# Kernel optimization log

Hardware: AMD Instinct MI355X
Metric: run time of the kernel (lower is better)

Reference implementation:

```python
import math
import jax, jax.numpy as jnp
import numpy as np

B, T, D, H = 2, 2048, 1024, 16
HD = D // H
LN_EPS = 1e-5


def new_gelu(x):
    c = math.sqrt(2.0 / math.pi)
    return 0.5 * x * (1.0 + jnp.tanh(c * (x + 0.044715 * x * x * x)))


def layer_norm(x, w, b):
    mu = jnp.mean(x, axis=-1, keepdims=True)
    var = jnp.var(x, axis=-1, keepdims=True)
    return (x - mu) * jax.lax.rsqrt(var + LN_EPS) * w + b


def setup_inputs() -> dict:
    key = jax.random.key(0)
    ks = jax.random.split(key, 9)
    s = 0.02
    return {
        "x": jax.random.normal(ks[0], (B, T, D), jnp.float32),
        "wq": jax.random.normal(ks[1], (D, D), jnp.float32) * s,
        "wk": jax.random.normal(ks[2], (D, D), jnp.float32) * s,
        "wv": jax.random.normal(ks[3], (D, D), jnp.float32) * s,
        "Er": jax.random.normal(ks[4], (H, T, HD), jnp.float32),
        "fc1_w": jax.random.normal(ks[5], (4 * D, D), jnp.float32) * s,
        "fc1_b": jax.random.normal(ks[6], (4 * D,), jnp.float32) * s,
        "fc2_w": jax.random.normal(ks[7], (D, 4 * D), jnp.float32) * s,
        "fc2_b": jax.random.normal(ks[8], (D,), jnp.float32) * s,
        "ln1_w": jnp.ones((D,), jnp.float32),
        "ln1_b": jnp.zeros((D,), jnp.float32),
        "ln2_w": jnp.ones((D,), jnp.float32),
        "ln2_b": jnp.zeros((D,), jnp.float32),
    }


def rel_attention(x, wq, wk, wv, Er):
    b, t, c = x.shape
    # torch nn.Linear: y = x @ W^T  (weights stored [out, in])
    q = (x @ wq.T).reshape(b, t, H, HD).transpose(0, 2, 1, 3)  # [B,H,T,HD]
    k = (x @ wk.T).reshape(b, t, H, HD).transpose(0, 2, 1, 3)
    v = (x @ wv.T).reshape(b, t, H, HD).transpose(0, 2, 1, 3)

    raw_attn = jnp.einsum("bhqd,bhkd->bhqk", q, k)  # [B,H,T,T]
    # relative-position logits + skew trick
    srel = jnp.einsum("bhqd,hrd->bhqr", q, Er[:, -t:, :])  # [B,H,T,T]
    srel = jnp.pad(srel, ((0, 0), (0, 0), (0, 0), (1, 0)))  # [B,H,T,T+1]
    srel = srel.reshape(b, H, t + 1, t)[:, :, 1:, :]  # skewed [B,H,T,T]

    attn = (raw_attn + srel) * (1.0 / math.sqrt(HD))
    causal = jnp.tril(jnp.ones((t, t), bool))
    attn = jnp.where(causal[None, None], attn, -jnp.inf)
    attn = jax.nn.softmax(attn, axis=-1)

    y = jnp.einsum("bhqk,bhkd->bhqd", attn, v)
    return y.transpose(0, 2, 1, 3).reshape(b, t, c)


def reference(x, wq, wk, wv, Er, fc1_w, fc1_b, fc2_w, fc2_b, ln1_w, ln1_b, ln2_w, ln2_b):
    x = x + rel_attention(layer_norm(x, ln1_w, ln1_b), wq, wk, wv, Er)
    h = layer_norm(x, ln2_w, ln2_b)
    h = new_gelu(h @ fc1_w.T + fc1_b)
    x = x + (h @ fc2_w.T + fc2_b)
    return x
```

## Files before the change

kernel.cpp:

```cpp
#include <hip/hip_runtime.h>
#include <hip/hip_bf16.h>

#define Bb 2
#define Tt 2048
#define Dd 1024
#define Hh 16

typedef short s16x8 __attribute__((ext_vector_type(8)));
typedef float f32x4 __attribute__((ext_vector_type(4)));
typedef unsigned short u16;
typedef short mfma_in_t __attribute__((ext_vector_type(8)));

typedef const __attribute__((address_space(1))) void gvoid;
typedef __attribute__((address_space(3))) void lvoid;

__device__ inline u16 f2bf(float f) {
  union { float f; unsigned u; } v; v.f = f;
  unsigned r = v.u + 0x7FFF + ((v.u >> 16) & 1);
  return (u16)(r >> 16);
}
__device__ inline u16 f2bf_t(float f) {
  return (u16)(__builtin_bit_cast(unsigned, f) >> 16);
}
__device__ inline float bf2f(u16 v) {
  return __builtin_bit_cast(float, (unsigned)v << 16);
}

__device__ inline f32x4 MFMA(s16x8 a, s16x8 b, f32x4 c) {
  return __builtin_amdgcn_mfma_f32_16x16x32_bf16(
      __builtin_bit_cast(mfma_in_t, a), __builtin_bit_cast(mfma_in_t, b), c, 0, 0, 0);
}

__global__ __launch_bounds__(256) void ln_kernel(const float* __restrict__ x,
    const float* __restrict__ w, const float* __restrict__ b, u16* __restrict__ out) {
  int row = blockIdx.x;
  const float4 v = ((const float4*)(x + (size_t)row * Dd))[threadIdx.x];
  float s = v.x + v.y + v.z + v.w;
  float sq = v.x * v.x + v.y * v.y + v.z * v.z + v.w * v.w;
#pragma unroll
  for (int off = 32; off; off >>= 1) { s += __shfl_down(s, off); sq += __shfl_down(sq, off); }
  __shared__ float red[8];
  int wid = threadIdx.x >> 6;
  if ((threadIdx.x & 63) == 0) { red[wid] = s; red[4 + wid] = sq; }
  __syncthreads();
  s = red[0] + red[1] + red[2] + red[3];
  sq = red[4] + red[5] + red[6] + red[7];
  float mean = s * (1.0f / Dd);
  float var = sq * (1.0f / Dd) - mean * mean;
  float rs = rsqrtf(var + 1e-5f);
  float4 wv = ((const float4*)w)[threadIdx.x];
  float4 bv = ((const float4*)b)[threadIdx.x];
  ushort4 o = make_ushort4(f2bf((v.x - mean) * rs * wv.x + bv.x),
                           f2bf((v.y - mean) * rs * wv.y + bv.y),
                           f2bf((v.z - mean) * rs * wv.z + bv.z),
                           f2bf((v.w - mean) * rs * wv.w + bv.w));
  ((ushort4*)(out + (size_t)row * Dd))[threadIdx.x] = o;
}

__global__ __launch_bounds__(256) void cvt6_kernel(
    const float* __restrict__ s0, u16* __restrict__ d0,
    const float* __restrict__ s1, u16* __restrict__ d1,
    const float* __restrict__ s2, u16* __restrict__ d2,
    const float* __restrict__ s3, u16* __restrict__ d3,
    const float* __restrict__ s4, u16* __restrict__ d4,
    const float* __restrict__ s5, u16* __restrict__ d5) {
  int blk = blockIdx.x;
  const float* s; u16* d; int base;
  if (blk < 1024)      { s = s0; d = d0; base = blk; }
  else if (blk < 1536) { s = s1; d = d1; base = blk - 1024; }
  else if (blk < 2048) { s = s2; d = d2; base = blk - 1536; }
  else if (blk < 2560) { s = s3; d = d3; base = blk - 2048; }
  else if (blk < 4608) { s = s4; d = d4; base = blk - 2560; }
  else                 { s = s5; d = d5; base = blk - 4608; }
  int i = base * 256 + threadIdx.x;
  const float4* p = (const float4*)s;
  float4 a = p[i * 2], b2 = p[i * 2 + 1];
  ((ushort4*)d)[i * 2]     = make_ushort4(f2bf(a.x), f2bf(a.y), f2bf(a.z), f2bf(a.w));
  ((ushort4*)d)[i * 2 + 1] = make_ushort4(f2bf(b2.x), f2bf(b2.y), f2bf(b2.z), f2bf(b2.w));
}

template <int EPI, int BN, int BK>
__global__ __launch_bounds__(256, 2) void gemm_bt(
    const u16* __restrict__ A, const u16* __restrict__ W,
    const float* __restrict__ bias, const float* __restrict__ res,
    void* __restrict__ outp, u16* __restrict__ vtout, int K, int ldout) {
  constexpr int MR = (BN == 128) ? 4 : 2;
  constexpr int LPR = BK / 8;
  constexpr int RPC = 512 / BK;
  constexpr int CA = (128 * BK) / 512;
  constexpr int CB = (BN * BK) / 512;
  __shared__ u16 As[2][128 * BK];
  __shared__ u16 Bs[2][BN * BK];
  const int bm = blockIdx.x, bn = blockIdx.y;
  const int t = threadIdx.x, lane = t & 63, w = t >> 6;
  const int l15 = lane & 15, l16 = lane >> 4;
  const int rbase = (BN == 128) ? (w >> 1) * 64 : w * 32;
  const int cbase = (BN == 128) ? (w & 1) * 64 : 0;
  f32x4 acc[MR][4] = {};
  const u16* Abase = A + (size_t)(bm * 128) * K;
  const u16* Wbase = W + (size_t)(bn * BN) * K;
  const int frow = lane / LPR;
  const int fcol = ((lane & (LPR - 1)) ^ (frow & (LPR - 1))) * 8;
#define GEMM_STAGE(k0_, nb_)                                                              \
  _Pragma("unroll")                                                                       \
  for (int i = 0; i < CA / 4; i++) {                                                      \
    int q = w * (CA / 4) + i;                                                             \
    int row = q * RPC + frow;                                                             \
    __builtin_amdgcn_global_load_lds((gvoid*)(Abase + (size_t)row * K + (k0_) + fcol),    \
                                     (lvoid*)&As[nb_][q * 512], 16, 0, 0);                \
  }                                                                                       \
  _Pragma("unroll")                                                                       \
  for (int i = 0; i < CB / 4; i++) {                                                      \
    int q = w * (CB / 4) + i;                                                             \
    int row = q * RPC + frow;                                                             \
    __builtin_amdgcn_global_load_lds((gvoid*)(Wbase + (size_t)row * K + (k0_) + fcol),    \
                                     (lvoid*)&Bs[nb_][q * 512], 16, 0, 0);                \
  }
  GEMM_STAGE(0, 0);
  __syncthreads();
  int cur = 0;
  for (int k0 = 0; k0 < K; k0 += BK) {
    if (k0 + BK < K) { GEMM_STAGE(k0 + BK, cur ^ 1); }
#pragma unroll
    for (int kk = 0; kk < BK / 32; kk++) {
      s16x8 af[MR], bfr[4];
#pragma unroll
      for (int rt = 0; rt < MR; rt++) {
        int ar = rbase + rt * 16 + l15;
        af[rt] = *(const s16x8*)&As[cur][ar * BK + (((kk * 4 + l16) ^ (ar & (LPR - 1))) * 8)];
      }
#pragma unroll
      for (int ct = 0; ct < 4; ct++) {
        int br = cbase + ct * 16 + l15;
        bfr[ct] = *(const s16x8*)&Bs[cur][br * BK + (((kk * 4 + l16) ^ (br & (LPR - 1))) * 8)];
      }
#pragma unroll
      for (int rt = 0; rt < MR; rt++)
#pragma unroll
        for (int ct = 0; ct < 4; ct++)
          acc[rt][ct] = MFMA(af[rt], bfr[ct], acc[rt][ct]);
    }
    __syncthreads();
    cur ^= 1;
  }
  if constexpr (EPI == 0) {
    const int wcb = bn * BN + cbase;
    if (wcb >= 2 * Dd) {
      const int hb = (wcb - 2 * Dd) >> 6;
      const int bb = bm >> 4;
      u16* vb = vtout + ((size_t)(bb * Hh + hb) * 64) * Tt;
#pragma unroll
      for (int rt = 0; rt < MR; rt++) {
        const int tok0v = (bm & 15) * 128 + rbase + l16 * 4 + rt * 16;
#pragma unroll
        for (int ct = 0; ct < 4; ct++) {
          const int dd = ct * 16 + l15;
          ushort4 pk = make_ushort4(f2bf(acc[rt][ct][0]), f2bf(acc[rt][ct][1]),
                                    f2bf(acc[rt][ct][2]), f2bf(acc[rt][ct][3]));
          *(ushort4*)(vb + (size_t)dd * Tt + tok0v) = pk;
        }
      }
      return;
    }
  }
  const int rg0 = bm * 128 + rbase + l16 * 4;
  const int cg0 = bn * BN + cbase + l15;
#pragma unroll
  for (int rt = 0; rt < MR; rt++) {
#pragma unroll
    for (int ct = 0; ct < 4; ct++) {
#pragma unroll
      for (int j = 0; j < 4; j++) {
        int r = rg0 + rt * 16 + j;
        int c = cg0 + ct * 16;
        float v = acc[rt][ct][j];
        if constexpr (EPI == 0) {
          ((u16*)outp)[(size_t)r * ldout + c] = f2bf(v);
        } else if constexpr (EPI == 1) {
          v += bias[c];
          float u = 0.7978845608f * (v + 0.044715f * v * v * v);
          float th = 1.0f - 2.0f / (__expf(2.0f * u) + 1.0f);
          ((u16*)outp)[(size_t)r * ldout + c] = f2bf(0.5f * v * (1.0f + th));
        } else {
          v += bias[c] + res[(size_t)r * Dd + c];
          ((float*)outp)[(size_t)r * ldout + c] = v;
        }
      }
    }
  }
}

__global__ __launch_bounds__(256, 2) void attn_kernel(
    const u16* __restrict__ qkv,
    const u16* __restrict__ erb,
    const u16* __restrict__ vt,
    const float* __restrict__ x,
    float* __restrict__ x2) {
  __shared__ u16 Ksm[64 * 72];
  __shared__ u16 Vsm[64 * 72];
  __shared__ u16 Esm[128 * 72];
  __shared__ u16 Gsm[4][16 * 85];
  const int lin = (int)blockIdx.x + 16 * ((int)blockIdx.y + 16 * (int)blockIdx.z);
  const int swz = (lin & 7) * 64 + (lin >> 3);
  const int pairid = swz & 15;
  const int h = (swz >> 4) & 15;
  const int b = swz >> 8;
  const int t = threadIdx.x, lane = t & 63, w = t >> 6;
  const int l15 = lane & 15, l16 = lane >> 4;
  u16* gw = Gsm[w];
  u16* Pw = gw;
  const int tr = t >> 3, tc = (t & 7) * 8;
  const u16* kbase = qkv + ((size_t)b * Tt) * 3072 + Dd + h * 64;
  const u16* vbase = vt + ((size_t)(b * Hh + h) * 64) * Tt;
  const u16* ebase = erb + (size_t)h * Tt * 64;
  s16x8 kR0, kR1, vR0, vR1, eR0, eR1, eR2, eR3;
#define ATTN_PREFETCH(kjn_, qin_)                                              \
  {                                                                            \
    const int kjn = (kjn_);                                                    \
    kR0 = *(const s16x8*)(kbase + (size_t)(kjn + tr) * 3072 + tc);             \
    kR1 = *(const s16x8*)(kbase + (size_t)(kjn + 32 + tr) * 3072 + tc);        \
    vR0 = *(const s16x8*)(vbase + (size_t)tr * Tt + kjn + tc);                 \
    vR1 = *(const s16x8*)(vbase + (size_t)(32 + tr) * Tt + kjn + tc);          \
    const int rlo = Tt - 64 - (qin_) + kjn;                                    \
    int g0 = rlo + tr;          g0 = g0 > Tt - 1 ? Tt - 1 : g0;                \
    int g1 = rlo + 32 + tr;     g1 = g1 > Tt - 1 ? Tt - 1 : g1;                \
    int g2 = rlo + 64 + tr;     g2 = g2 > Tt - 1 ? Tt - 1 : g2;                \
    int g3 = rlo + 96 + tr;     g3 = g3 > Tt - 1 ? Tt - 1 : g3;                \
    eR0 = *(const s16x8*)(ebase + (size_t)g0 * 64 + tc);                       \
    eR1 = *(const s16x8*)(ebase + (size_t)g1 * 64 + tc);                       \
    eR2 = *(const s16x8*)(ebase + (size_t)g2 * 64 + tc);                       \
    eR3 = *(const s16x8*)(ebase + (size_t)g3 * 64 + tc);                       \
  }
  for (int pass = 0; pass < 2; ++pass) {
    const int qt = pass ? 31 - pairid : pairid;
    const int qi = qt * 64;
    const int nt = qt + 1;
    const int qb = qi + w * 16;
    const u16* qp = qkv + (size_t)(b * Tt + qb + l15) * 3072 + h * 64 + l16 * 8;
    const s16x8 qf0 = *(const s16x8*)qp;
    const s16x8 qf1 = *(const s16x8*)(qp + 32);
    f32x4 o_acc[4] = {};
    float l_lane[4] = {0.f, 0.f, 0.f, 0.f};
    if (pass == 0) { ATTN_PREFETCH(0, qi); }
    for (int it = 0; it < nt; ++it) {
      const int kj = it * 64;
      *(s16x8*)&Ksm[tr * 72 + tc] = kR0;
      *(s16x8*)&Ksm[(32 + tr) * 72 + tc] = kR1;
      *(s16x8*)&Vsm[tr * 72 + tc] = vR0;
      *(s16x8*)&Vsm[(32 + tr) * 72 + tc] = vR1;
      *(s16x8*)&Esm[tr * 72 + tc] = eR0;
      *(s16x8*)&Esm[(32 + tr) * 72 + tc] = eR1;
      *(s16x8*)&Esm[(64 + tr) * 72 + tc] = eR2;
      *(s16x8*)&Esm[(96 + tr) * 72 + tc] = eR3;
      __syncthreads();
      if (it + 1 < nt) {
        ATTN_PREFETCH(kj + 64, qi);
      } else if (pass == 0) {
        ATTN_PREFETCH(0, (31 - pairid) * 64);
      }
      f32x4 s_acc[4] = {};
#pragma unroll
      for (int ct = 0; ct < 4; ct++) {
        int col = ct * 16 + l15;
        s16x8 k0 = *(const s16x8*)&Ksm[col * 72 + l16 * 8];
        s16x8 k1 = *(const s16x8*)&Ksm[col * 72 + 32 + l16 * 8];
        s_acc[ct] = MFMA(qf1, k1, MFMA(qf0, k0, s_acc[ct]));
      }
      const int ub = 48 - 16 * w;
#pragma unroll
      for (int gt = 0; gt < 5; gt++) {
        int ur = ub + gt * 16 + l15;
        s16x8 e0 = *(const s16x8*)&Esm[ur * 72 + l16 * 8];
        s16x8 e1 = *(const s16x8*)&Esm[ur * 72 + 32 + l16 * 8];
        f32x4 z = {};
        f32x4 ga = MFMA(qf1, e1, MFMA(qf0, e0, z));
#pragma unroll
        for (int j = 0; j < 4; j++) gw[(l16 * 4 + j) * 85 + gt * 16 + l15] = f2bf_t(ga[j]);
      }
      float p[4][4];
      if (kj + 63 <= qb) {
#pragma unroll
        for (int j = 0; j < 4; j++) {
          const int di = l16 * 4 + j;
          float lacc = 0.f;
#pragma unroll
          for (int ct = 0; ct < 4; ct++) {
            int dj = ct * 16 + l15;
            float pe = __expf((s_acc[ct][j] + bf2f(gw[di * 85 + dj - di + 15])) * 0.125f - 8.0f);
            p[j][ct] = pe;
            lacc += pe;
          }
          l_lane[j] += lacc;
        }
      } else {
#pragma unroll
        for (int j = 0; j < 4; j++) {
          const int di = l16 * 4 + j;
          const int ig = qb + di;
          float lacc = 0.f;
#pragma unroll
          for (int ct = 0; ct < 4; ct++) {
            int dj = ct * 16 + l15;
            float pe = 0.f;
            if (kj + dj <= ig)
              pe = __expf((s_acc[ct][j] + bf2f(gw[di * 85 + dj - di + 15])) * 0.125f - 8.0f);
            p[j][ct] = pe;
            lacc += pe;
          }
          l_lane[j] += lacc;
        }
      }
#pragma unroll
      for (int j = 0; j < 4; j++)
#pragma unroll
        for (int ct = 0; ct < 4; ct++)
          Pw[(l16 * 4 + j) * 72 + ct * 16 + l15] = f2bf_t(p[j][ct]);
      s16x8 pa0 = *(const s16x8*)&Pw[l15 * 72 + l16 * 8];
      s16x8 pa1 = *(const s16x8*)&Pw[l15 * 72 + 32 + l16 * 8];
#pragma unroll
      for (int g = 0; g < 4; g++) {
        s16x8 v0 = *(const s16x8*)&Vsm[(g * 16 + l15) * 72 + l16 * 8];
        s16x8 v1 = *(const s16x8*)&Vsm[(g * 16 + l15) * 72 + 32 + l16 * 8];
        o_acc[g] = MFMA(pa1, v1, MFMA(pa0, v0, o_acc[g]));
      }
      __syncthreads();
    }
#pragma unroll
    for (int j = 0; j < 4; j++) {
#pragma unroll
      for (int o = 1; o < 16; o <<= 1) l_lane[j] += __shfl_xor(l_lane[j], o);
    }
#pragma unroll
    for (int g = 0; g < 4; g++)
#pragma unroll
      for (int j = 0; j < 4; j++) {
        int r = qb + l16 * 4 + j;
        int c = h * 64 + g * 16 + l15;
        size_t idx = (size_t)(b * Tt + r) * Dd + c;
        x2[idx] = x[idx] + o_acc[g][j] / l_lane[j];
      }
  }
}

extern "C" void kernel_launch(void* const* d_in, const int* in_sizes, int n_in,
                              void* d_out, int out_size, void* d_ws, size_t ws_size,
                              hipStream_t stream) {
  const float* x     = (const float*)d_in[0];
  const float* wq    = (const float*)d_in[1];
  const float* wk    = (const float*)d_in[2];
  const float* wv    = (const float*)d_in[3];
  const float* Er    = (const float*)d_in[4];
  const float* fc1_w = (const float*)d_in[5];
  const float* fc1_b = (const float*)d_in[6];
  const float* fc2_w = (const float*)d_in[7];
  const float* fc2_b = (const float*)d_in[8];
  const float* ln1_w = (const float*)d_in[9];
  const float* ln1_b = (const float*)d_in[10];
  const float* ln2_w = (const float*)d_in[11];
  const float* ln2_b = (const float*)d_in[12];

  const size_t MB = 1024 * 1024;
  char* ws = (char*)d_ws;
  u16*   h1   = (u16*)ws;
  u16*   qkv  = (u16*)(ws + 8 * MB);
  u16*   vtb  = (u16*)(ws + 32 * MB);
  u16*   erb  = (u16*)(ws + 40 * MB);
  float* x2   = (float*)(ws + 44 * MB);
  u16*   wqkb = (u16*)(ws + 60 * MB);
  u16*   f1b  = (u16*)(ws + 66 * MB);
  u16*   f2b  = (u16*)(ws + 74 * MB);
  u16*   a1   = (u16*)(ws + 8 * MB);
  float* out  = (float*)d_out;

  ln_kernel<<<dim3(Bb * Tt), 256, 0, stream>>>(x, ln1_w, ln1_b, h1);
  cvt6_kernel<<<dim3(6656), 256, 0, stream>>>(
      Er, erb, wq, wqkb, wk, wqkb + 1024 * 1024, wv, wqkb + 2 * 1024 * 1024,
      fc1_w, f1b, fc2_w, f2b);
  gemm_bt<0, 128, 32><<<dim3(32, 24), 256, 0, stream>>>(h1, wqkb, nullptr, nullptr, qkv, vtb, Dd, 3072);
  attn_kernel<<<dim3(16, 16, 2), 256, 0, stream>>>(qkv, erb, vtb, x, x2);
  ln_kernel<<<dim3(Bb * Tt), 256, 0, stream>>>(x2, ln2_w, ln2_b, h1);
  gemm_bt<1, 128, 32><<<dim3(32, 32), 256, 0, stream>>>(h1, f1b, fc1_b, nullptr, a1, nullptr, Dd, 4096);
  gemm_bt<2, 64, 64><<<dim3(32, 16), 256, 0, stream>>>(a1, f2b, fc2_b, x2, out, nullptr, 4096, Dd);
}
```

Baseline: 238.8 us.

## Double-buffer K/V in LDS and read relative-position rows directly from global

K and V tiles are now double-buffered in shared memory, which removes the trailing barrier so each iteration has a single __syncthreads. The relative-position Er tile is no longer staged through LDS. Each wave loads its own 5x16 Er rows straight from global (cached) memory into MFMA operands. This cuts LDS traffic and footprint and drops one barrier per iteration, at the cost of more uncoalesced global/L2 loads that sit on the critical path just before the MFMAs.

```diff
diff --git a/kernel.cpp b/kernel.cpp
--- a/kernel.cpp
+++ b/kernel.cpp
@@ -196,9 +196,8 @@
     const u16* __restrict__ vt,
     const float* __restrict__ x,
     float* __restrict__ x2) {
-  __shared__ u16 Ksm[64 * 72];
-  __shared__ u16 Vsm[64 * 72];
-  __shared__ u16 Esm[128 * 72];
+  __shared__ u16 Ksm[2][64 * 72];
+  __shared__ u16 Vsm[2][64 * 72];
   __shared__ u16 Gsm[4][16 * 85];
   const int lin = (int)blockIdx.x + 16 * ((int)blockIdx.y + 16 * (int)blockIdx.z);
   const int swz = (lin & 7) * 64 + (lin >> 3);
@@ -213,24 +212,17 @@
   const u16* kbase = qkv + ((size_t)b * Tt) * 3072 + Dd + h * 64;
   const u16* vbase = vt + ((size_t)(b * Hh + h) * 64) * Tt;
   const u16* ebase = erb + (size_t)h * Tt * 64;
-  s16x8 kR0, kR1, vR0, vR1, eR0, eR1, eR2, eR3;
-#define ATTN_PREFETCH(kjn_, qin_)                                              \
+  s16x8 kR0, kR1, vR0, vR1;
+#define ATTN_PREFETCH(kjn_)                                                    \
   {                                                                            \
     const int kjn = (kjn_);                                                    \
     kR0 = *(const s16x8*)(kbase + (size_t)(kjn + tr) * 3072 + tc);             \
     kR1 = *(const s16x8*)(kbase + (size_t)(kjn + 32 + tr) * 3072 + tc);        \
     vR0 = *(const s16x8*)(vbase + (size_t)tr * Tt + kjn + tc);                 \
     vR1 = *(const s16x8*)(vbase + (size_t)(32 + tr) * Tt + kjn + tc);          \
-    const int rlo = Tt - 64 - (qin_) + kjn;                                    \
-    int g0 = rlo + tr;          g0 = g0 > Tt - 1 ? Tt - 1 : g0;                \
-    int g1 = rlo + 32 + tr;     g1 = g1 > Tt - 1 ? Tt - 1 : g1;                \
-    int g2 = rlo + 64 + tr;     g2 = g2 > Tt - 1 ? Tt - 1 : g2;                \
-    int g3 = rlo + 96 + tr;     g3 = g3 > Tt - 1 ? Tt - 1 : g3;                \
-    eR0 = *(const s16x8*)(ebase + (size_t)g0 * 64 + tc);                       \
-    eR1 = *(const s16x8*)(ebase + (size_t)g1 * 64 + tc);                       \
-    eR2 = *(const s16x8*)(ebase + (size_t)g2 * 64 + tc);                       \
-    eR3 = *(const s16x8*)(ebase + (size_t)g3 * 64 + tc);                       \
-  }
+  }
+  int pbuf = 0;
+  ATTN_PREFETCH(0);
   for (int pass = 0; pass < 2; ++pass) {
     const int qt = pass ? 31 - pairid : pairid;
     const int qi = qt * 64;
@@ -241,37 +233,35 @@
     const s16x8 qf1 = *(const s16x8*)(qp + 32);
     f32x4 o_acc[4] = {};
     float l_lane[4] = {0.f, 0.f, 0.f, 0.f};
-    if (pass == 0) { ATTN_PREFETCH(0, qi); }
     for (int it = 0; it < nt; ++it) {
       const int kj = it * 64;
-      *(s16x8*)&Ksm[tr * 72 + tc] = kR0;
-      *(s16x8*)&Ksm[(32 + tr) * 72 + tc] = kR1;
-      *(s16x8*)&Vsm[tr * 72 + tc] = vR0;
-      *(s16x8*)&Vsm[(32 + tr) * 72 + tc] = vR1;
-      *(s16x8*)&Esm[tr * 72 + tc] = eR0;
-      *(s16x8*)&Esm[(32 + tr) * 72 + tc] = eR1;
-      *(s16x8*)&Esm[(64 + tr) * 72 + tc] = eR2;
-      *(s16x8*)&Esm[(96 + tr) * 72 + tc] = eR3;
+      const int cb = pbuf & 1;
+      *(s16x8*)&Ksm[cb][tr * 72 + tc] = kR0;
+      *(s16x8*)&Ksm[cb][(32 + tr) * 72 + tc] = kR1;
+      *(s16x8*)&Vsm[cb][tr * 72 + tc] = vR0;
+      *(s16x8*)&Vsm[cb][(32 + tr) * 72 + tc] = vR1;
       __syncthreads();
       if (it + 1 < nt) {
-        ATTN_PREFETCH(kj + 64, qi);
+        ATTN_PREFETCH(kj + 64);
       } else if (pass == 0) {
-        ATTN_PREFETCH(0, (31 - pairid) * 64);
+        ATTN_PREFETCH(0);
       }
       f32x4 s_acc[4] = {};
 #pragma unroll
       for (int ct = 0; ct < 4; ct++) {
         int col = ct * 16 + l15;
-        s16x8 k0 = *(const s16x8*)&Ksm[col * 72 + l16 * 8];
-        s16x8 k1 = *(const s16x8*)&Ksm[col * 72 + 32 + l16 * 8];
+        s16x8 k0 = *(const s16x8*)&Ksm[cb][col * 72 + l16 * 8];
+        s16x8 k1 = *(const s16x8*)&Ksm[cb][col * 72 + 32 + l16 * 8];
         s_acc[ct] = MFMA(qf1, k1, MFMA(qf0, k0, s_acc[ct]));
       }
-      const int ub = 48 - 16 * w;
+      const int rb2 = Tt - 16 - qb + kj;
 #pragma unroll
       for (int gt = 0; gt < 5; gt++) {
-        int ur = ub + gt * 16 + l15;
-        s16x8 e0 = *(const s16x8*)&Esm[ur * 72 + l16 * 8];
-        s16x8 e1 = *(const s16x8*)&Esm[ur * 72 + 32 + l16 * 8];
+        int r = rb2 + gt * 16 + l15;
+        r = (r > Tt - 1) ? Tt - 1 : r;
+        const u16* ep = ebase + (size_t)r * 64 + l16 * 8;
+        s16x8 e0 = *(const s16x8*)ep;
+        s16x8 e1 = *(const s16x8*)(ep + 32);
         f32x4 z = {};
         f32x4 ga = MFMA(qf1, e1, MFMA(qf0, e0, z));
 #pragma unroll
@@ -319,11 +309,11 @@
       s16x8 pa1 = *(const s16x8*)&Pw[l15 * 72 + 32 + l16 * 8];
 #pragma unroll
       for (int g = 0; g < 4; g++) {
-        s16x8 v0 = *(const s16x8*)&Vsm[(g * 16 + l15) * 72 + l16 * 8];
-        s16x8 v1 = *(const s16x8*)&Vsm[(g * 16 + l15) * 72 + 32 + l16 * 8];
+        s16x8 v0 = *(const s16x8*)&Vsm[cb][(g * 16 + l15) * 72 + l16 * 8];
+        s16x8 v1 = *(const s16x8*)&Vsm[cb][(g * 16 + l15) * 72 + 32 + l16 * 8];
         o_acc[g] = MFMA(pa1, v1, MFMA(pa0, v0, o_acc[g]));
       }
-      __syncthreads();
+      ++pbuf;
     }
 #pragma unroll
     for (int j = 0; j < 4; j++) {
```

Measured after the change: 250.6 us. 4.9% more time.
